# Kernel tuning notes

Hardware: AMD Instinct MI355X
Metric: run time of the kernel (lower is better)

Reference implementation:

```python
import jax, jax.numpy as jnp
import numpy as np

N_ROWS = 1048576   # total clips
D = 128            # embedding dim
N_SEG = 2048       # number of videos (segments)
SEG_LEN = N_ROWS // N_SEG


def setup_inputs() -> dict:
    key = jax.random.key(0)
    k1, k2 = jax.random.split(key)
    clip_remap = jax.random.normal(k1, (N_ROWS, D), dtype=jnp.float32)
    clip_emb = jax.random.normal(k2, (N_ROWS, D), dtype=jnp.float32)
    # ragged segment lengths; constant here, must sum to N_ROWS
    num_list = jnp.full((N_SEG,), SEG_LEN, dtype=jnp.int32)
    return {"clip_remap": clip_remap, "clip_emb": clip_emb, "num_list": num_list}


def reference(clip_remap, clip_emb, num_list):
    n = clip_remap.shape[0]
    diff = clip_remap - clip_emb                       # [N, D]
    score_sub = jnp.sqrt(jnp.sum(diff * diff, axis=1))  # [N] per-row L2 distance
    # segment id per row from ragged lengths (static total length -> jit ok)
    seg_ids = jnp.repeat(jnp.arange(num_list.shape[0]), num_list,
                         total_repeat_length=n)        # [N]
    denom = num_list[seg_ids].astype(score_sub.dtype)  # [N] segment length per row
    return jnp.sum(score_sub / denom)                  # scalar loss
```

## Files before the change

kernel.cpp:

```cpp
#include <hip/hip_runtime.h>
#include <math.h>


__global__ void zero_out_kernel(float* out) {
    out[0] = 0.0f;
}

__global__ __launch_bounds__(256) void euclid_loss_kernel(
    const float* __restrict__ remap,
    const float* __restrict__ emb,
    const int*   __restrict__ num_list,
    float*       __restrict__ out,
    int n_seg)
{
    const int seg  = blockIdx.x;
    const int tid  = threadIdx.x;
    const int wid  = tid >> 6;
    const int lane = tid & 63;
    const int sub  = lane >> 5;
    const int l32  = lane & 31;

    __shared__ int   s_red[4];
    __shared__ int   s_start, s_len;
    __shared__ float s_acc[4];

    int partial = 0;
    for (int i = tid; i < seg; i += 256) partial += num_list[i];
    #pragma unroll
    for (int off = 32; off >= 1; off >>= 1) partial += __shfl_down(partial, off, 64);
    if (lane == 0) s_red[wid] = partial;
    __syncthreads();
    if (tid == 0) {
        s_start = s_red[0] + s_red[1] + s_red[2] + s_red[3];
        s_len   = num_list[seg];
    }
    __syncthreads();
    const int seg_start = s_start;
    const int seg_len   = s_len;

    float acc = 0.0f;
    for (int r = wid * 2 + sub; r < seg_len; r += 8) {
        const long long row = (long long)(seg_start + r);
        const float4 va = *((const float4*)(remap + row * 128) + l32);
        const float4 vb = *((const float4*)(emb   + row * 128) + l32);
        const float dx = va.x - vb.x;
        const float dy = va.y - vb.y;
        const float dz = va.z - vb.z;
        const float dw = va.w - vb.w;
        float s = dx * dx + dy * dy + dz * dz + dw * dw;
        s += __shfl_xor(s, 1, 64);
        s += __shfl_xor(s, 2, 64);
        s += __shfl_xor(s, 4, 64);
        s += __shfl_xor(s, 8, 64);
        s += __shfl_xor(s, 16, 64);
        if (l32 == 0) acc += sqrtf(s);
    }

    #pragma unroll
    for (int off = 32; off >= 1; off >>= 1) acc += __shfl_down(acc, off, 64);
    if (lane == 0) s_acc[wid] = acc;
    __syncthreads();
    if (tid == 0) {
        const float total = s_acc[0] + s_acc[1] + s_acc[2] + s_acc[3];
        atomicAdd(out, total / (float)seg_len);
    }
}

extern "C" void kernel_launch(void* const* d_in, const int* in_sizes, int n_in,
                              void* d_out, int out_size, void* d_ws, size_t ws_size,
                              hipStream_t stream) {
    const float* remap    = (const float*)d_in[0];
    const float* emb      = (const float*)d_in[1];
    const int*   num_list = (const int*)d_in[2];
    float*       out      = (float*)d_out;

    const int n_seg = in_sizes[2];

    zero_out_kernel<<<1, 1, 0, stream>>>(out);
    euclid_loss_kernel<<<n_seg, 256, 0, stream>>>(remap, emb, num_list, out, n_seg);
}
```

Before: 197.8 us.

## Precompute segment offsets in prep kernel; unroll row loop with nontemporal loads

Moves the per-block prefix sum over num_list into a single-block prep kernel that writes segment starts to workspace and zeroes the output. Without it, every block rescans up to 2048 ints before it does any work. The main loop now handles two rows per iteration, which gives more independent loads in flight, and uses nontemporal loads to stream data that is read only once. The cost is a serial single-block prep kernel with a log-step scan ahead of the main kernel, and reliance on the workspace buffer.

New measurement: 176.9 us. -10.6%, faster.

```diff
diff --git a/kernel.cpp b/kernel.cpp
--- a/kernel.cpp
+++ b/kernel.cpp
@@ -1,17 +1,45 @@
 #include <hip/hip_runtime.h>
 #include <math.h>
 
+typedef float v4f __attribute__((ext_vector_type(4)));
 
-__global__ void zero_out_kernel(float* out) {
-    out[0] = 0.0f;
+__global__ __launch_bounds__(256) void prep_kernel(const int* __restrict__ num_list,
+                                                   int n_seg,
+                                                   float* __restrict__ out,
+                                                   int* __restrict__ seg_start) {
+    __shared__ int s_sum[256];
+    const int tid = threadIdx.x;
+    const int C  = (n_seg + 255) >> 8;
+    const int lo = tid * C;
+    const int hi = (lo + C < n_seg) ? (lo + C) : n_seg;
+
+    int sum = 0;
+    for (int i = lo; i < hi; ++i) sum += num_list[i];
+    s_sum[tid] = sum;
+    __syncthreads();
+
+    for (int off = 1; off < 256; off <<= 1) {
+        int v   = s_sum[tid];
+        int add = (tid >= off) ? s_sum[tid - off] : 0;
+        __syncthreads();
+        s_sum[tid] = v + add;
+        __syncthreads();
+    }
+
+    int excl = (tid == 0) ? 0 : s_sum[tid - 1];
+    for (int i = lo; i < hi; ++i) {
+        seg_start[i] = excl;
+        excl += num_list[i];
+    }
+    if (tid == 0) out[0] = 0.0f;
 }
 
 __global__ __launch_bounds__(256) void euclid_loss_kernel(
     const float* __restrict__ remap,
     const float* __restrict__ emb,
     const int*   __restrict__ num_list,
-    float*       __restrict__ out,
-    int n_seg)
+    const int*   __restrict__ seg_start_arr,
+    float*       __restrict__ out)
 {
     const int seg  = blockIdx.x;
     const int tid  = threadIdx.x;
@@ -20,49 +48,50 @@
     const int sub  = lane >> 5;
     const int l32  = lane & 31;
 
-    __shared__ int   s_red[4];
-    __shared__ int   s_start, s_len;
-    __shared__ float s_acc[4];
+    const int seg_start = seg_start_arr[seg];
+    const int seg_len   = num_list[seg];
 
-    int partial = 0;
-    for (int i = tid; i < seg; i += 256) partial += num_list[i];
-    #pragma unroll
-    for (int off = 32; off >= 1; off >>= 1) partial += __shfl_down(partial, off, 64);
-    if (lane == 0) s_red[wid] = partial;
-    __syncthreads();
-    if (tid == 0) {
-        s_start = s_red[0] + s_red[1] + s_red[2] + s_red[3];
-        s_len   = num_list[seg];
-    }
-    __syncthreads();
-    const int seg_start = s_start;
-    const int seg_len   = s_len;
+    const v4f* __restrict__ pa = (const v4f*)remap;
+    const v4f* __restrict__ pb = (const v4f*)emb;
 
     float acc = 0.0f;
-    for (int r = wid * 2 + sub; r < seg_len; r += 8) {
+    int r = wid * 2 + sub;
+
+    for (; r + 8 < seg_len; r += 16) {
+        const long long row0 = (long long)(seg_start + r);
+        const long long row1 = row0 + 8;
+        const v4f a0 = __builtin_nontemporal_load(pa + row0 * 32 + l32);
+        const v4f b0 = __builtin_nontemporal_load(pb + row0 * 32 + l32);
+        const v4f a1 = __builtin_nontemporal_load(pa + row1 * 32 + l32);
+        const v4f b1 = __builtin_nontemporal_load(pb + row1 * 32 + l32);
+        const v4f d0 = a0 - b0;
+        const v4f d1 = a1 - b1;
+        float s0 = d0[0]*d0[0] + d0[1]*d0[1] + d0[2]*d0[2] + d0[3]*d0[3];
+        float s1 = d1[0]*d1[0] + d1[1]*d1[1] + d1[2]*d1[2] + d1[3]*d1[3];
+        #pragma unroll
+        for (int m = 1; m <= 16; m <<= 1) s0 += __shfl_xor(s0, m, 64);
+        #pragma unroll
+        for (int m = 1; m <= 16; m <<= 1) s1 += __shfl_xor(s1, m, 64);
+        if (l32 == 0) acc += sqrtf(s0) + sqrtf(s1);
+    }
+    for (; r < seg_len; r += 8) {
         const long long row = (long long)(seg_start + r);
-        const float4 va = *((const float4*)(remap + row * 128) + l32);
-        const float4 vb = *((const float4*)(emb   + row * 128) + l32);
-        const float dx = va.x - vb.x;
-        const float dy = va.y - vb.y;
-        const float dz = va.z - vb.z;
-        const float dw = va.w - vb.w;
-        float s = dx * dx + dy * dy + dz * dz + dw * dw;
-        s += __shfl_xor(s, 1, 64);
-        s += __shfl_xor(s, 2, 64);
-        s += __shfl_xor(s, 4, 64);
-        s += __shfl_xor(s, 8, 64);
-        s += __shfl_xor(s, 16, 64);
+        const v4f a = __builtin_nontemporal_load(pa + row * 32 + l32);
+        const v4f b = __builtin_nontemporal_load(pb + row * 32 + l32);
+        const v4f d = a - b;
+        float s = d[0]*d[0] + d[1]*d[1] + d[2]*d[2] + d[3]*d[3];
+        #pragma unroll
+        for (int m = 1; m <= 16; m <<= 1) s += __shfl_xor(s, m, 64);
         if (l32 == 0) acc += sqrtf(s);
     }
 
     #pragma unroll
     for (int off = 32; off >= 1; off >>= 1) acc += __shfl_down(acc, off, 64);
+    __shared__ float s_acc[4];
     if (lane == 0) s_acc[wid] = acc;
     __syncthreads();
     if (tid == 0) {
-        const float total = s_acc[0] + s_acc[1] + s_acc[2] + s_acc[3];
-        atomicAdd(out, total / (float)seg_len);
+        atomicAdd(out, (s_acc[0] + s_acc[1] + s_acc[2] + s_acc[3]) / (float)seg_len);
     }
 }
 
@@ -73,9 +102,10 @@
     const float* emb      = (const float*)d_in[1];
     const int*   num_list = (const int*)d_in[2];
     float*       out      = (float*)d_out;
+    int*         seg_start = (int*)d_ws;
 
     const int n_seg = in_sizes[2];
 
-    zero_out_kernel<<<1, 1, 0, stream>>>(out);
-    euclid_loss_kernel<<<n_seg, 256, 0, stream>>>(remap, emb, num_list, out, n_seg);
+    prep_kernel<<<1, 256, 0, stream>>>(num_list, n_seg, out, seg_start);
+    euclid_loss_kernel<<<n_seg, 256, 0, stream>>>(remap, emb, num_list, seg_start, out);
 }
```
